# Kernel optimization log

Hardware: AMD Instinct MI355X
Metric: run time of the kernel (lower is better)

## Reference

```python
import jax, jax.numpy as jnp
import numpy as np

D_MODEL = 128
NHEAD = 8
HEAD_DIM = D_MODEL // NHEAD  # 16
NUM_LAYERS = 7
NUM_LABELS = 2
N_NODES = 10000
N_EDGES = 160000
NEG_SLOPE = 0.2  # GATv2Conv default negative_slope


def setup_inputs() -> dict:
    key = jax.random.key(0)
    ks = jax.random.split(key, 10)
    s = 1.0 / np.sqrt(D_MODEL)
    inp = {}
    inp["x"] = jax.random.normal(ks[0], (N_NODES, D_MODEL), dtype=jnp.float32)
    inp["edge_index"] = jax.random.randint(ks[1], (2, N_EDGES), 0, N_NODES, dtype=jnp.int64)
    inp["nchunks"] = 8  # uniform extra chunk size -> chunk = NUM_LABELS + 8 = 10
    # per-layer GATv2 params, stacked on a leading layer axis
    inp["Wl"] = jax.random.normal(ks[2], (NUM_LAYERS, D_MODEL, NHEAD * HEAD_DIM), dtype=jnp.float32) * s
    inp["bl"] = jnp.zeros((NUM_LAYERS, NHEAD * HEAD_DIM), dtype=jnp.float32)
    inp["Wr"] = jax.random.normal(ks[3], (NUM_LAYERS, D_MODEL, NHEAD * HEAD_DIM), dtype=jnp.float32) * s
    inp["br"] = jnp.zeros((NUM_LAYERS, NHEAD * HEAD_DIM), dtype=jnp.float32)
    inp["att"] = jax.random.normal(ks[4], (NUM_LAYERS, NHEAD, HEAD_DIM), dtype=jnp.float32) * s
    inp["bias"] = jnp.zeros((NUM_LAYERS, NHEAD * HEAD_DIM), dtype=jnp.float32)
    # split head: Linear(d_model, 1)
    inp["w_head"] = jax.random.normal(ks[5], (D_MODEL, 1), dtype=jnp.float32) * s
    inp["b_head"] = jnp.zeros((1,), dtype=jnp.float32)
    return inp


def _gatv2_layer(x, src, dst, Wl, bl, Wr, br, att, bias):
    # GATv2: e_ij = a^T LeakyReLU(W_l x_j + W_r x_i); alpha = segment-softmax over dst; out_i = sum alpha * W_l x_j
    N = x.shape[0]
    xl = (x @ Wl + bl).reshape(N, NHEAD, HEAD_DIM)
    xr = (x @ Wr + br).reshape(N, NHEAD, HEAD_DIM)
    z = jax.nn.leaky_relu(xl[src] + xr[dst], NEG_SLOPE)          # [E, H, D]
    e = jnp.einsum('ehd,hd->eh', z, att)                          # [E, H]
    emax = jax.ops.segment_max(e, dst, num_segments=N)            # [N, H]
    ex = jnp.exp(e - emax[dst])
    denom = jax.ops.segment_sum(ex, dst, num_segments=N)          # [N, H]
    alpha = ex / (denom[dst] + 1e-16)                             # [E, H]
    out = jax.ops.segment_sum(alpha[..., None] * xl[src], dst, num_segments=N)  # [N, H, D]
    return out.reshape(N, NHEAD * HEAD_DIM) + bias


def reference(x, edge_index, nchunks, Wl, bl, Wr, br, att, bias, w_head, b_head):
    N = x.shape[0]
    loop = jnp.arange(N, dtype=edge_index.dtype)  # GATv2Conv add_self_loops=True
    src = jnp.concatenate([edge_index[0], loop])
    dst = jnp.concatenate([edge_index[1], loop])
    for i in range(NUM_LAYERS):
        x = _gatv2_layer(x, src, dst, Wl[i], bl[i], Wr[i], br[i], att[i], bias[i])
    # uniform split of size (NUM_LABELS + nchunks); keep first NUM_LABELS rows of each chunk
    chunk = NUM_LABELS + int(nchunks)
    xs = x.reshape(-1, chunk, D_MODEL)[:, :NUM_LABELS]            # [n_chunks, num_labels, d]
    out = (xs @ w_head + b_head)[..., 0]                          # [n_chunks, num_labels]
    return out
```

## Files before the change

kernel.cpp:

```cpp
#include <hip/hip_runtime.h>
#include <math.h>

typedef __attribute__((ext_vector_type(8))) short bf16x8;
typedef __attribute__((ext_vector_type(4))) float f32x4;

#define WFRAG (16 * 4 * 64 * 8)


__device__ inline int detect_is64(const int* __restrict__ ei) {
    int is64 = 1;
#pragma unroll
    for (int k = 1; k < 16; k += 2) is64 &= (ei[k] == 0);
    return is64;
}

__device__ inline void split1(float f, short& hi, short& lo) {
    unsigned u = __float_as_uint(f);
    hi = (short)(u >> 16);
    float fl = f - __uint_as_float(u & 0xffff0000u);
    lo = (short)(__float_as_uint(fl) >> 16);
}

__device__ inline void cvt8(const float4& a, const float4& b, bf16x8& hi, bf16x8& lo) {
    float f[8] = {a.x, a.y, a.z, a.w, b.x, b.y, b.z, b.w};
#pragma unroll
    for (int j = 0; j < 8; j++) {
        unsigned u = __float_as_uint(f[j]);
        hi[j] = (short)(u >> 16);
        float fl = f[j] - __uint_as_float(u & 0xffff0000u);
        lo[j] = (short)(__float_as_uint(fl) >> 16);
    }
}


__global__ __launch_bounds__(256) void prologue(const float* __restrict__ Wl,
                                                const float* __restrict__ Wr,
                                                short* __restrict__ Whi,
                                                short* __restrict__ Wlo,
                                                const float4* __restrict__ x4,
                                                short* __restrict__ cvH,
                                                short* __restrict__ cvL,
                                                const int* __restrict__ ei,
                                                int* __restrict__ deg,
                                                int N, int E) {
    __shared__ float Wt[128][17];
    int b = blockIdx.x, t = threadIdx.x;
    if (b < 112) {
        int l = b >> 4;
        int tile = b & 15;
        int c0 = tile * 16;
        const float* Wsrc = (c0 < 128) ? Wl + (size_t)l * 16384 : Wr + (size_t)l * 16384;
        int cbase = (c0 < 128) ? c0 : c0 - 128;
#pragma unroll
        for (int it = 0; it < 8; it++) {
            int idx = it * 256 + t;
            int k = idx >> 4, c = idx & 15;
            Wt[k][c] = Wsrc[(size_t)k * 128 + cbase + c];
        }
        __syncthreads();
        int kt = t >> 6, lane = t & 63, q = (lane >> 4), cl = lane & 15;
        bf16x8 hi, lo;
#pragma unroll
        for (int j = 0; j < 8; j++) {
            short h, lw;
            split1(Wt[kt * 32 + q * 8 + j][cl], h, lw);
            hi[j] = h; lo[j] = lw;
        }
        size_t off = ((((size_t)l * 16 + tile) * 4 + kt) * 64 + lane) * 8;
        *(bf16x8*)(Whi + off) = hi;
        *(bf16x8*)(Wlo + off) = lo;
        return;
    }
    int rb = b - 112;
    int RB = gridDim.x - 112;
    int n8 = N * 16;
    for (int id = rb * 256 + t; id < n8; id += RB * 256) {
        float4 a = x4[2 * id];
        float4 bb = x4[2 * id + 1];
        bf16x8 h, lw;
        cvt8(a, bb, h, lw);
        *(bf16x8*)(cvH + (size_t)id * 8) = h;
        *(bf16x8*)(cvL + (size_t)id * 8) = lw;
    }
    int is64 = detect_is64(ei);
    for (int e = rb * 256 + t; e < E; e += RB * 256) {
        long long pos = (long long)E + e;
        int d = ei[is64 ? 2 * pos : pos];
        if ((unsigned)d < (unsigned)N) atomicAdd(&deg[d], 1);
    }
}


__global__ __launch_bounds__(512, 1) void scan_gemm0(const int* __restrict__ deg,
                                                     int* __restrict__ offp,
                                                     int* __restrict__ cur, int N,
                                                     const short* __restrict__ xhi,
                                                     const short* __restrict__ xlo,
                                                     const short* __restrict__ WhiL,
                                                     const short* __restrict__ WloL,
                                                     const float* __restrict__ blv,
                                                     const float* __restrict__ brv,
                                                     float* __restrict__ xl,
                                                     float* __restrict__ xr,
                                                     int ntiles) {
    __shared__ int wsum[8];
    int t = threadIdx.x;
    if (blockIdx.x == 0) {
        int per = (N + 511) >> 9;
        int b0 = t * per;
        int s = 0;
        for (int k = 0; k < per; k++) {
            int idx = b0 + k;
            if (idx < N) s += deg[idx];
        }
        int lane = t & 63, w = t >> 6;
        int v = s;
#pragma unroll
        for (int o = 1; o < 64; o <<= 1) {
            int u = __shfl_up(v, o, 64);
            if (lane >= o) v += u;
        }
        if (lane == 63) wsum[w] = v;
        __syncthreads();
        if (t == 0) {
            int r = 0;
#pragma unroll
            for (int j = 0; j < 8; j++) { int xx = wsum[j]; wsum[j] = r; r += xx; }
            offp[N] = r;
        }
        __syncthreads();
        int run = v - s + wsum[w];
        for (int k = 0; k < per; k++) {
            int idx = b0 + k;
            if (idx < N) {
                offp[idx] = run;
                cur[idx] = run;
                run += deg[idx];
            }
        }
        return;
    }

    int w = t >> 6, lane = t & 63, q = lane >> 4, cl = lane & 15;

    bf16x8 Bh[2][4], Bl[2][4];
    float biasv[2];
    float* op[2];
    int colc[2];
#pragma unroll
    for (int nt = 0; nt < 2; nt++) {
        int tile = w * 2 + nt;
        int col = tile * 16 + cl;
        if (col < 128) { biasv[nt] = blv[col]; op[nt] = xl; colc[nt] = col; }
        else           { biasv[nt] = brv[col - 128]; op[nt] = xr; colc[nt] = col - 128; }
#pragma unroll
        for (int kt = 0; kt < 4; kt++) {
            size_t o = (((size_t)tile * 4 + kt) * 64 + lane) * 8;
            Bh[nt][kt] = *(const bf16x8*)(WhiL + o);
            Bl[nt][kt] = *(const bf16x8*)(WloL + o);
        }
    }

    for (int rt = blockIdx.x - 1; rt < ntiles; rt += gridDim.x - 1) {
        int row = rt * 16 + cl;
        if (row >= N) row = N - 1;
        const short* ph = xhi + (size_t)row * 128 + q * 8;
        const short* pl = xlo + (size_t)row * 128 + q * 8;
        bf16x8 AH[4], AL[4];
#pragma unroll
        for (int kt = 0; kt < 4; kt++) {
            AH[kt] = *(const bf16x8*)(ph + kt * 32);
            AL[kt] = *(const bf16x8*)(pl + kt * 32);
        }

        f32x4 acc0 = {0.f, 0.f, 0.f, 0.f}, acc1 = {0.f, 0.f, 0.f, 0.f};
#pragma unroll
        for (int kt = 0; kt < 4; kt++) {
            acc0 = __builtin_amdgcn_mfma_f32_16x16x32_bf16(AH[kt], Bh[0][kt], acc0, 0, 0, 0);
            acc1 = __builtin_amdgcn_mfma_f32_16x16x32_bf16(AH[kt], Bh[1][kt], acc1, 0, 0, 0);
            acc0 = __builtin_amdgcn_mfma_f32_16x16x32_bf16(AL[kt], Bh[0][kt], acc0, 0, 0, 0);
            acc1 = __builtin_amdgcn_mfma_f32_16x16x32_bf16(AL[kt], Bh[1][kt], acc1, 0, 0, 0);
            acc0 = __builtin_amdgcn_mfma_f32_16x16x32_bf16(AH[kt], Bl[0][kt], acc0, 0, 0, 0);
            acc1 = __builtin_amdgcn_mfma_f32_16x16x32_bf16(AH[kt], Bl[1][kt], acc1, 0, 0, 0);
        }

#pragma unroll
        for (int nt = 0; nt < 2; nt++) {
            f32x4 a = nt ? acc1 : acc0;
#pragma unroll
            for (int r = 0; r < 4; r++) {
                int orow = rt * 16 + q * 4 + r;
                if (orow < N) op[nt][(size_t)orow * 128 + colc[nt]] = a[r] + biasv[nt];
            }
        }
    }
}

__global__ void fill_kernel(const int* __restrict__ ei, int E, int N,
                            int* __restrict__ cur, int* __restrict__ esrc) {
    int e = blockIdx.x * blockDim.x + threadIdx.x;
    if (e >= E) return;
    int is64 = detect_is64(ei);
    long long spos = e, dpos = (long long)E + e;
    int s = ei[is64 ? 2 * spos : spos];
    int d = ei[is64 ? 2 * dpos : dpos];
    if ((unsigned)d >= (unsigned)N || (unsigned)s >= (unsigned)N) return;
    int p = atomicAdd(&cur[d], 1);
    esrc[p] = s;
}


__device__ inline void agg_node(int i, int sub, int cl,
                                const float4* __restrict__ xl4, const float4* __restrict__ xr4,
                                const int* __restrict__ off, const int* __restrict__ esrc,
                                float4 atA, float4 atB, float4 bA, float4 bB,
                                float4& oA, float4& oB) {
    float4 xrA = xr4[(size_t)i * 32 + 2 * cl];
    float4 xrB = xr4[(size_t)i * 32 + 2 * cl + 1];
    int start = off[i];
    int total = off[i + 1] - start + 1;
    int groups = (total + 3) >> 2;

    int k0 = sub;
    int s0 = (k0 < total) ? ((k0 == 0) ? i : esrc[start + k0 - 1]) : i;
    int k1 = 4 + sub;
    int s1 = (k1 < total) ? esrc[start + k1 - 1] : i;
    float4 v0A = xl4[(size_t)s0 * 32 + 2 * cl];
    float4 v0B = xl4[(size_t)s0 * 32 + 2 * cl + 1];
    int k2 = 8 + sub;
    int s2 = (k2 < total) ? esrc[start + k2 - 1] : i;
    float4 v1A = xl4[(size_t)s1 * 32 + 2 * cl];
    float4 v1B = xl4[(size_t)s1 * 32 + 2 * cl + 1];

    float s = 0.f;
    float4 aA = make_float4(0.f, 0.f, 0.f, 0.f);
    float4 aB = make_float4(0.f, 0.f, 0.f, 0.f);

    for (int g = 0; g < groups; g++) {
        int k3 = 4 * (g + 3) + sub;
        int s3 = (k3 < total) ? esrc[start + k3 - 1] : i;
        float4 v2A = xl4[(size_t)s2 * 32 + 2 * cl];
        float4 v2B = xl4[(size_t)s2 * 32 + 2 * cl + 1];

        int kc = 4 * g + sub;
        int valid = kc < total;
        float z0 = v0A.x + xrA.x, z1 = v0A.y + xrA.y, z2 = v0A.z + xrA.z, z3 = v0A.w + xrA.w;
        float z4 = v0B.x + xrB.x, z5 = v0B.y + xrB.y, z6 = v0B.z + xrB.z, z7 = v0B.w + xrB.w;
        z0 = (z0 > 0.f) ? z0 : 0.2f * z0;
        z1 = (z1 > 0.f) ? z1 : 0.2f * z1;
        z2 = (z2 > 0.f) ? z2 : 0.2f * z2;
        z3 = (z3 > 0.f) ? z3 : 0.2f * z3;
        z4 = (z4 > 0.f) ? z4 : 0.2f * z4;
        z5 = (z5 > 0.f) ? z5 : 0.2f * z5;
        z6 = (z6 > 0.f) ? z6 : 0.2f * z6;
        z7 = (z7 > 0.f) ? z7 : 0.2f * z7;
        float p = z0 * atA.x + z1 * atA.y + z2 * atA.z + z3 * atA.w
                + z4 * atB.x + z5 * atB.y + z6 * atB.z + z7 * atB.w;
        p += __shfl_xor(p, 1, 64);
        p = fminf(fmaxf(p, -80.f), 80.f);
        float wgt = valid ? __expf(p) : 0.f;
        s += wgt;
        aA.x += wgt * v0A.x; aA.y += wgt * v0A.y; aA.z += wgt * v0A.z; aA.w += wgt * v0A.w;
        aB.x += wgt * v0B.x; aB.y += wgt * v0B.y; aB.z += wgt * v0B.z; aB.w += wgt * v0B.w;

        v0A = v1A; v0B = v1B;
        v1A = v2A; v1B = v2B;
        s2 = s3;
    }

#pragma unroll
    for (int o = 16; o <= 32; o <<= 1) {
        s += __shfl_xor(s, o, 64);
        aA.x += __shfl_xor(aA.x, o, 64); aA.y += __shfl_xor(aA.y, o, 64);
        aA.z += __shfl_xor(aA.z, o, 64); aA.w += __shfl_xor(aA.w, o, 64);
        aB.x += __shfl_xor(aB.x, o, 64); aB.y += __shfl_xor(aB.y, o, 64);
        aB.z += __shfl_xor(aB.z, o, 64); aB.w += __shfl_xor(aB.w, o, 64);
    }
    float inv = 1.f / (s + 1e-16f);
    oA.x = aA.x * inv + bA.x; oA.y = aA.y * inv + bA.y;
    oA.z = aA.z * inv + bA.z; oA.w = aA.w * inv + bA.w;
    oB.x = aB.x * inv + bB.x; oB.y = aB.y * inv + bB.y;
    oB.z = aB.z * inv + bB.z; oB.w = aB.w * inv + bB.w;
}


__global__ __launch_bounds__(512, 1) void agg_gemm(const float4* __restrict__ xl4,
                                                   const float4* __restrict__ xr4,
                                                   const int* __restrict__ off,
                                                   const int* __restrict__ esrc,
                                                   const float4* __restrict__ att4,
                                                   const float4* __restrict__ bias4,
                                                   const short* __restrict__ WhiL,
                                                   const short* __restrict__ WloL,
                                                   const float* __restrict__ blv,
                                                   const float* __restrict__ brv,
                                                   float* __restrict__ xlo_out,
                                                   float* __restrict__ xro_out,
                                                   int N) {
    __shared__ __align__(16) short hiL[32 * 136];
    __shared__ __align__(16) short loL[32 * 136];
    int t = threadIdx.x;
    int w = t >> 6, lane = t & 63, sub = lane >> 4, cl = lane & 15, q = lane >> 4;
    int base = blockIdx.x * 32;

    float4 atA = att4[2 * cl];
    float4 atB = att4[2 * cl + 1];
    float4 bA = bias4[2 * cl], bB = bias4[2 * cl + 1];

    for (int j = 0; j < 4; j++) {
        int i = base + w * 4 + j;
        if (i < N) {
            float4 oA, oB;
            agg_node(i, sub, cl, xl4, xr4, off, esrc, atA, atB, bA, bB, oA, oB);
            if (sub == 0) {
                bf16x8 h, lw;
                cvt8(oA, oB, h, lw);
                int r = w * 4 + j;
                *(bf16x8*)&hiL[r * 136 + cl * 8] = h;
                *(bf16x8*)&loL[r * 136 + cl * 8] = lw;
            }
        }
    }
    __syncthreads();

    bf16x8 Bh[2][4], Bl[2][4];
    float biasv[2];
    float* op[2];
    int cc[2];
#pragma unroll
    for (int tt = 0; tt < 2; tt++) {
        int tile = w * 2 + tt;
        int col = tile * 16 + cl;
        if (col < 128) { biasv[tt] = blv[col]; op[tt] = xlo_out; cc[tt] = col; }
        else           { biasv[tt] = brv[col - 128]; op[tt] = xro_out; cc[tt] = col - 128; }
#pragma unroll
        for (int kt = 0; kt < 4; kt++) {
            size_t o = (((size_t)tile * 4 + kt) * 64 + lane) * 8;
            Bh[tt][kt] = *(const bf16x8*)(WhiL + o);
            Bl[tt][kt] = *(const bf16x8*)(WloL + o);
        }
    }

#pragma unroll
    for (int m = 0; m < 2; m++) {
        bf16x8 Ah[4], Al[4];
#pragma unroll
        for (int kt = 0; kt < 4; kt++) {
            Ah[kt] = *(const bf16x8*)&hiL[(m * 16 + cl) * 136 + kt * 32 + q * 8];
            Al[kt] = *(const bf16x8*)&loL[(m * 16 + cl) * 136 + kt * 32 + q * 8];
        }
#pragma unroll
        for (int tt = 0; tt < 2; tt++) {
            f32x4 acc = {0.f, 0.f, 0.f, 0.f};
#pragma unroll
            for (int kt = 0; kt < 4; kt++) {
                acc = __builtin_amdgcn_mfma_f32_16x16x32_bf16(Ah[kt], Bh[tt][kt], acc, 0, 0, 0);
                acc = __builtin_amdgcn_mfma_f32_16x16x32_bf16(Al[kt], Bh[tt][kt], acc, 0, 0, 0);
                acc = __builtin_amdgcn_mfma_f32_16x16x32_bf16(Ah[kt], Bl[tt][kt], acc, 0, 0, 0);
            }
#pragma unroll
            for (int r = 0; r < 4; r++) {
                int row = base + m * 16 + q * 4 + r;
                if (row < N) op[tt][(size_t)row * 128 + cc[tt]] = acc[r] + biasv[tt];
            }
        }
    }
}


__global__ __launch_bounds__(256) void gat_agg_head(const float4* __restrict__ xl4,
                                                    const float4* __restrict__ xr4,
                                                    const int* __restrict__ off,
                                                    const int* __restrict__ esrc,
                                                    const float4* __restrict__ att4,
                                                    const float4* __restrict__ bias4,
                                                    const float4* __restrict__ wh4,
                                                    const float* __restrict__ bh,
                                                    const int* __restrict__ nch,
                                                    float* __restrict__ out,
                                                    int n_out, int N) {
    int lane = threadIdx.x & 63;
    int sub = lane >> 4;
    int cl = lane & 15;
    int i = blockIdx.x * 4 + (threadIdx.x >> 6);
    if (i >= N) return;
    float4 atA = att4[2 * cl];
    float4 atB = att4[2 * cl + 1];
    float4 bA = bias4[2 * cl], bB = bias4[2 * cl + 1];
    float4 oA, oB;
    agg_node(i, sub, cl, xl4, xr4, off, esrc, atA, atB, bA, bB, oA, oB);
    if (sub == 0) {
        int chunk = 2 + nch[0];
        int r = i % chunk;
        if (r < 2) {
            float4 wa = wh4[2 * cl], wb = wh4[2 * cl + 1];
            float p = oA.x * wa.x + oA.y * wa.y + oA.z * wa.z + oA.w * wa.w
                    + oB.x * wb.x + oB.y * wb.y + oB.z * wb.z + oB.w * wb.w;
#pragma unroll
            for (int o = 1; o <= 8; o <<= 1) p += __shfl_xor(p, o, 64);
            if (cl == 0) {
                int b = (i / chunk) * 2 + r;
                if (b < n_out) out[b] = p + bh[0];
            }
        }
    }
}


extern "C" void kernel_launch(void* const* d_in, const int* in_sizes, int n_in,
                              void* d_out, int out_size, void* d_ws, size_t ws_size,
                              hipStream_t stream) {
    const float* x0 = (const float*)d_in[0];
    const int* ei = (const int*)d_in[1];
    const int* nchunks = (const int*)d_in[2];
    const float* Wl = (const float*)d_in[3];
    const float* bl = (const float*)d_in[4];
    const float* Wr = (const float*)d_in[5];
    const float* br = (const float*)d_in[6];
    const float* att = (const float*)d_in[7];
    const float* bias = (const float*)d_in[8];
    const float* wh = (const float*)d_in[9];
    const float* bh = (const float*)d_in[10];

    const int D = 128;
    int N = in_sizes[0] / D;
    int E = in_sizes[1] / 2;
    int ntiles = (N + 15) / 16;

    size_t fN = (size_t)N * D;
    float* xlA = (float*)d_ws;
    float* xrA = xlA + fN;
    float* xlB = xrA + fN;
    float* xrB = xlB + fN;
    short* cvH0 = (short*)(xrB + fN);
    short* cvL0 = cvH0 + fN;
    short* Whi = cvL0 + fN;
    short* Wlo = Whi + 7 * (size_t)WFRAG;
    int* deg = (int*)(Wlo + 7 * (size_t)WFRAG);
    int* off = deg + N;
    int* cur = off + N + 1;
    int* esrc = cur + N;

    hipMemsetAsync(deg, 0, (size_t)N * sizeof(int), stream);
    prologue<<<112 + 640, 256, 0, stream>>>(Wl, Wr, Whi, Wlo, (const float4*)x0,
                                            cvH0, cvL0, ei, deg, N, E);
    scan_gemm0<<<257, 512, 0, stream>>>(deg, off, cur, N, cvH0, cvL0, Whi, Wlo,
                                        bl, br, xlA, xrA, ntiles);
    fill_kernel<<<(E + 255) / 256, 256, 0, stream>>>(ei, E, N, cur, esrc);

    int ablocks = (N + 31) / 32;
    for (int l = 0; l < 6; l++) {
        const float* rxl = (l % 2 == 0) ? xlA : xlB;
        const float* rxr = (l % 2 == 0) ? xrA : xrB;
        float* wxl = (l % 2 == 0) ? xlB : xlA;
        float* wxr = (l % 2 == 0) ? xrB : xrA;
        agg_gemm<<<ablocks, 512, 0, stream>>>((const float4*)rxl, (const float4*)rxr, off, esrc,
                                              (const float4*)(att + (size_t)l * D),
                                              (const float4*)(bias + (size_t)l * D),
                                              Whi + (size_t)(l + 1) * WFRAG,
                                              Wlo + (size_t)(l + 1) * WFRAG,
                                              bl + (size_t)(l + 1) * D,
                                              br + (size_t)(l + 1) * D,
                                              wxl, wxr, N);
    }

    gat_agg_head<<<(N + 3) / 4, 256, 0, stream>>>((const float4*)xlA, (const float4*)xrA,
                                                  off, esrc,
                                                  (const float4*)(att + 6 * (size_t)D),
                                                  (const float4*)(bias + 6 * (size_t)D),
                                                  (const float4*)wh, bh, nchunks,
                                                  (float*)d_out, out_size, N);
}
```

Baseline: 273.8 us.

## Aggregate one node per half-wave and shrink fused agg-GEMM blocks to sixteen rows

```diff
diff --git a/kernel.cpp b/kernel.cpp
--- a/kernel.cpp
+++ b/kernel.cpp
@@ -210,81 +210,109 @@
 }
 
 
-__device__ inline void agg_node(int i, int sub, int cl,
-                                const float4* __restrict__ xl4, const float4* __restrict__ xr4,
-                                const int* __restrict__ off, const int* __restrict__ esrc,
-                                float4 atA, float4 atB, float4 bA, float4 bB,
-                                float4& oA, float4& oB) {
-    float4 xrA = xr4[(size_t)i * 32 + 2 * cl];
-    float4 xrB = xr4[(size_t)i * 32 + 2 * cl + 1];
+__device__ inline void agg_node_hw(int i, int s, int f,
+                                   const float4* __restrict__ xl4,
+                                   const float4* __restrict__ xr4,
+                                   const int* __restrict__ off,
+                                   const int* __restrict__ esrc,
+                                   const float4* __restrict__ att4,
+                                   const float4* __restrict__ bias4,
+                                   float4 (&out)[4]) {
+    float4 xr0 = xr4[(size_t)i * 32 + f * 4 + 0];
+    float4 xr1 = xr4[(size_t)i * 32 + f * 4 + 1];
+    float4 xr2 = xr4[(size_t)i * 32 + f * 4 + 2];
+    float4 xr3 = xr4[(size_t)i * 32 + f * 4 + 3];
+    float4 at0 = att4[f * 4 + 0];
+    float4 at1 = att4[f * 4 + 1];
+    float4 at2 = att4[f * 4 + 2];
+    float4 at3 = att4[f * 4 + 3];
+
     int start = off[i];
     int total = off[i + 1] - start + 1;
     int groups = (total + 3) >> 2;
 
-    int k0 = sub;
+    int k0 = s;
     int s0 = (k0 < total) ? ((k0 == 0) ? i : esrc[start + k0 - 1]) : i;
-    int k1 = 4 + sub;
+    const float4* p0 = xl4 + (size_t)s0 * 32 + f * 4;
+    float4 a0 = p0[0], a1 = p0[1], a2 = p0[2], a3 = p0[3];
+    int k1 = 4 + s;
     int s1 = (k1 < total) ? esrc[start + k1 - 1] : i;
-    float4 v0A = xl4[(size_t)s0 * 32 + 2 * cl];
-    float4 v0B = xl4[(size_t)s0 * 32 + 2 * cl + 1];
-    int k2 = 8 + sub;
-    int s2 = (k2 < total) ? esrc[start + k2 - 1] : i;
-    float4 v1A = xl4[(size_t)s1 * 32 + 2 * cl];
-    float4 v1B = xl4[(size_t)s1 * 32 + 2 * cl + 1];
-
-    float s = 0.f;
-    float4 aA = make_float4(0.f, 0.f, 0.f, 0.f);
-    float4 aB = make_float4(0.f, 0.f, 0.f, 0.f);
+    const float4* p1 = xl4 + (size_t)s1 * 32 + f * 4;
+    float4 b0 = p1[0], b1 = p1[1], b2 = p1[2], b3 = p1[3];
+
+    float denom = 0.f;
+    float4 ac0 = make_float4(0.f, 0.f, 0.f, 0.f);
+    float4 ac1 = make_float4(0.f, 0.f, 0.f, 0.f);
+    float4 ac2 = make_float4(0.f, 0.f, 0.f, 0.f);
+    float4 ac3 = make_float4(0.f, 0.f, 0.f, 0.f);
 
     for (int g = 0; g < groups; g++) {
-        int k3 = 4 * (g + 3) + sub;
-        int s3 = (k3 < total) ? esrc[start + k3 - 1] : i;
-        float4 v2A = xl4[(size_t)s2 * 32 + 2 * cl];
-        float4 v2B = xl4[(size_t)s2 * 32 + 2 * cl + 1];
-
-        int kc = 4 * g + sub;
-        int valid = kc < total;
-        float z0 = v0A.x + xrA.x, z1 = v0A.y + xrA.y, z2 = v0A.z + xrA.z, z3 = v0A.w + xrA.w;
-        float z4 = v0B.x + xrB.x, z5 = v0B.y + xrB.y, z6 = v0B.z + xrB.z, z7 = v0B.w + xrB.w;
-        z0 = (z0 > 0.f) ? z0 : 0.2f * z0;
-        z1 = (z1 > 0.f) ? z1 : 0.2f * z1;
-        z2 = (z2 > 0.f) ? z2 : 0.2f * z2;
-        z3 = (z3 > 0.f) ? z3 : 0.2f * z3;
-        z4 = (z4 > 0.f) ? z4 : 0.2f * z4;
-        z5 = (z5 > 0.f) ? z5 : 0.2f * z5;
-        z6 = (z6 > 0.f) ? z6 : 0.2f * z6;
-        z7 = (z7 > 0.f) ? z7 : 0.2f * z7;
-        float p = z0 * atA.x + z1 * atA.y + z2 * atA.z + z3 * atA.w
-                + z4 * atB.x + z5 * atB.y + z6 * atB.z + z7 * atB.w;
-        p += __shfl_xor(p, 1, 64);
+        int k2 = (g + 2) * 4 + s;
+        int s2 = (k2 < total) ? esrc[start + k2 - 1] : i;
+        const float4* p2 = xl4 + (size_t)s2 * 32 + f * 4;
+        float4 c0 = p2[0], c1 = p2[1], c2 = p2[2], c3 = p2[3];
+
+        int valid = (g * 4 + s) < total;
+#define LK(zz) ((zz) > 0.f ? (zz) : 0.2f * (zz))
+        float p = 0.f, z;
+        z = LK(a0.x + xr0.x); p += z * at0.x;
+        z = LK(a0.y + xr0.y); p += z * at0.y;
+        z = LK(a0.z + xr0.z); p += z * at0.z;
+        z = LK(a0.w + xr0.w); p += z * at0.w;
+        z = LK(a1.x + xr1.x); p += z * at1.x;
+        z = LK(a1.y + xr1.y); p += z * at1.y;
+        z = LK(a1.z + xr1.z); p += z * at1.z;
+        z = LK(a1.w + xr1.w); p += z * at1.w;
+        z = LK(a2.x + xr2.x); p += z * at2.x;
+        z = LK(a2.y + xr2.y); p += z * at2.y;
+        z = LK(a2.z + xr2.z); p += z * at2.z;
+        z = LK(a2.w + xr2.w); p += z * at2.w;
+        z = LK(a3.x + xr3.x); p += z * at3.x;
+        z = LK(a3.y + xr3.y); p += z * at3.y;
+        z = LK(a3.z + xr3.z); p += z * at3.z;
+        z = LK(a3.w + xr3.w); p += z * at3.w;
+#undef LK
         p = fminf(fmaxf(p, -80.f), 80.f);
         float wgt = valid ? __expf(p) : 0.f;
-        s += wgt;
-        aA.x += wgt * v0A.x; aA.y += wgt * v0A.y; aA.z += wgt * v0A.z; aA.w += wgt * v0A.w;
-        aB.x += wgt * v0B.x; aB.y += wgt * v0B.y; aB.z += wgt * v0B.z; aB.w += wgt * v0B.w;
-
-        v0A = v1A; v0B = v1B;
-        v1A = v2A; v1B = v2B;
-        s2 = s3;
-    }
-
-#pragma unroll
-    for (int o = 16; o <= 32; o <<= 1) {
-        s += __shfl_xor(s, o, 64);
-        aA.x += __shfl_xor(aA.x, o, 64); aA.y += __shfl_xor(aA.y, o, 64);
-        aA.z += __shfl_xor(aA.z, o, 64); aA.w += __shfl_xor(aA.w, o, 64);
-        aB.x += __shfl_xor(aB.x, o, 64); aB.y += __shfl_xor(aB.y, o, 64);
-        aB.z += __shfl_xor(aB.z, o, 64); aB.w += __shfl_xor(aB.w, o, 64);
-    }
-    float inv = 1.f / (s + 1e-16f);
-    oA.x = aA.x * inv + bA.x; oA.y = aA.y * inv + bA.y;
-    oA.z = aA.z * inv + bA.z; oA.w = aA.w * inv + bA.w;
-    oB.x = aB.x * inv + bB.x; oB.y = aB.y * inv + bB.y;
-    oB.z = aB.z * inv + bB.z; oB.w = aB.w * inv + bB.w;
-}
-
-
-__global__ __launch_bounds__(512, 1) void agg_gemm(const float4* __restrict__ xl4,
+        denom += wgt;
+        ac0.x += wgt * a0.x; ac0.y += wgt * a0.y; ac0.z += wgt * a0.z; ac0.w += wgt * a0.w;
+        ac1.x += wgt * a1.x; ac1.y += wgt * a1.y; ac1.z += wgt * a1.z; ac1.w += wgt * a1.w;
+        ac2.x += wgt * a2.x; ac2.y += wgt * a2.y; ac2.z += wgt * a2.z; ac2.w += wgt * a2.w;
+        ac3.x += wgt * a3.x; ac3.y += wgt * a3.y; ac3.z += wgt * a3.z; ac3.w += wgt * a3.w;
+
+        a0 = b0; a1 = b1; a2 = b2; a3 = b3;
+        b0 = c0; b1 = c1; b2 = c2; b3 = c3;
+    }
+
+#pragma unroll
+    for (int o = 8; o <= 16; o <<= 1) {
+        denom += __shfl_xor(denom, o, 64);
+        ac0.x += __shfl_xor(ac0.x, o, 64); ac0.y += __shfl_xor(ac0.y, o, 64);
+        ac0.z += __shfl_xor(ac0.z, o, 64); ac0.w += __shfl_xor(ac0.w, o, 64);
+        ac1.x += __shfl_xor(ac1.x, o, 64); ac1.y += __shfl_xor(ac1.y, o, 64);
+        ac1.z += __shfl_xor(ac1.z, o, 64); ac1.w += __shfl_xor(ac1.w, o, 64);
+        ac2.x += __shfl_xor(ac2.x, o, 64); ac2.y += __shfl_xor(ac2.y, o, 64);
+        ac2.z += __shfl_xor(ac2.z, o, 64); ac2.w += __shfl_xor(ac2.w, o, 64);
+        ac3.x += __shfl_xor(ac3.x, o, 64); ac3.y += __shfl_xor(ac3.y, o, 64);
+        ac3.z += __shfl_xor(ac3.z, o, 64); ac3.w += __shfl_xor(ac3.w, o, 64);
+    }
+    float inv = 1.f / (denom + 1e-16f);
+    float4 bi0 = bias4[f * 4 + 0];
+    float4 bi1 = bias4[f * 4 + 1];
+    float4 bi2 = bias4[f * 4 + 2];
+    float4 bi3 = bias4[f * 4 + 3];
+    out[0].x = ac0.x * inv + bi0.x; out[0].y = ac0.y * inv + bi0.y;
+    out[0].z = ac0.z * inv + bi0.z; out[0].w = ac0.w * inv + bi0.w;
+    out[1].x = ac1.x * inv + bi1.x; out[1].y = ac1.y * inv + bi1.y;
+    out[1].z = ac1.z * inv + bi1.z; out[1].w = ac1.w * inv + bi1.w;
+    out[2].x = ac2.x * inv + bi2.x; out[2].y = ac2.y * inv + bi2.y;
+    out[2].z = ac2.z * inv + bi2.z; out[2].w = ac2.w * inv + bi2.w;
+    out[3].x = ac3.x * inv + bi3.x; out[3].y = ac3.y * inv + bi3.y;
+    out[3].z = ac3.z * inv + bi3.z; out[3].w = ac3.w * inv + bi3.w;
+}
+
+
+__global__ __launch_bounds__(512, 2) void agg_gemm(const float4* __restrict__ xl4,
                                                    const float4* __restrict__ xr4,
                                                    const int* __restrict__ off,
                                                    const int* __restrict__ esrc,
@@ -297,108 +325,99 @@
                                                    float* __restrict__ xlo_out,
                                                    float* __restrict__ xro_out,
                                                    int N) {
-    __shared__ __align__(16) short hiL[32 * 136];
-    __shared__ __align__(16) short loL[32 * 136];
+    __shared__ __align__(16) short hiL[16 * 136];
+    __shared__ __align__(16) short loL[16 * 136];
     int t = threadIdx.x;
-    int w = t >> 6, lane = t & 63, sub = lane >> 4, cl = lane & 15, q = lane >> 4;
-    int base = blockIdx.x * 32;
-
-    float4 atA = att4[2 * cl];
-    float4 atB = att4[2 * cl + 1];
-    float4 bA = bias4[2 * cl], bB = bias4[2 * cl + 1];
-
-    for (int j = 0; j < 4; j++) {
-        int i = base + w * 4 + j;
-        if (i < N) {
-            float4 oA, oB;
-            agg_node(i, sub, cl, xl4, xr4, off, esrc, atA, atB, bA, bB, oA, oB);
-            if (sub == 0) {
-                bf16x8 h, lw;
-                cvt8(oA, oB, h, lw);
-                int r = w * 4 + j;
-                *(bf16x8*)&hiL[r * 136 + cl * 8] = h;
-                *(bf16x8*)&loL[r * 136 + cl * 8] = lw;
-            }
+    int hw = t >> 5;
+    int u = t & 31, s = u >> 3, f = u & 7;
+    int base = blockIdx.x * 16;
+    int i = base + hw;
+
+    if (i < N) {
+        float4 o[4];
+        agg_node_hw(i, s, f, xl4, xr4, off, esrc, att4, bias4, o);
+        if (s == 0) {
+            bf16x8 h0, l0, h1, l1;
+            cvt8(o[0], o[1], h0, l0);
+            cvt8(o[2], o[3], h1, l1);
+            *(bf16x8*)&hiL[hw * 136 + f * 16] = h0;
+            *(bf16x8*)&hiL[hw * 136 + f * 16 + 8] = h1;
+            *(bf16x8*)&loL[hw * 136 + f * 16] = l0;
+            *(bf16x8*)&loL[hw * 136 + f * 16 + 8] = l1;
         }
     }
     __syncthreads();
 
-    bf16x8 Bh[2][4], Bl[2][4];
-    float biasv[2];
-    float* op[2];
-    int cc[2];
+    int w = t >> 6, lane = t & 63, q = lane >> 4, cl = lane & 15;
+    bf16x8 Ah[4], Al[4];
+#pragma unroll
+    for (int kt = 0; kt < 4; kt++) {
+        Ah[kt] = *(const bf16x8*)&hiL[cl * 136 + kt * 32 + q * 8];
+        Al[kt] = *(const bf16x8*)&loL[cl * 136 + kt * 32 + q * 8];
+    }
+
 #pragma unroll
     for (int tt = 0; tt < 2; tt++) {
         int tile = w * 2 + tt;
         int col = tile * 16 + cl;
-        if (col < 128) { biasv[tt] = blv[col]; op[tt] = xlo_out; cc[tt] = col; }
-        else           { biasv[tt] = brv[col - 128]; op[tt] = xro_out; cc[tt] = col - 128; }
+        f32x4 acc = {0.f, 0.f, 0.f, 0.f};
 #pragma unroll
         for (int kt = 0; kt < 4; kt++) {
             size_t o = (((size_t)tile * 4 + kt) * 64 + lane) * 8;
-            Bh[tt][kt] = *(const bf16x8*)(WhiL + o);
-            Bl[tt][kt] = *(const bf16x8*)(WloL + o);
-        }
-    }
-
-#pragma unroll
-    for (int m = 0; m < 2; m++) {
-        bf16x8 Ah[4], Al[4];
-#pragma unroll
-        for (int kt = 0; kt < 4; kt++) {
-            Ah[kt] = *(const bf16x8*)&hiL[(m * 16 + cl) * 136 + kt * 32 + q * 8];
-            Al[kt] = *(const bf16x8*)&loL[(m * 16 + cl) * 136 + kt * 32 + q * 8];
-        }
-#pragma unroll
-        for (int tt = 0; tt < 2; tt++) {
-            f32x4 acc = {0.f, 0.f, 0.f, 0.f};
-#pragma unroll
-            for (int kt = 0; kt < 4; kt++) {
-                acc = __builtin_amdgcn_mfma_f32_16x16x32_bf16(Ah[kt], Bh[tt][kt], acc, 0, 0, 0);
-                acc = __builtin_amdgcn_mfma_f32_16x16x32_bf16(Al[kt], Bh[tt][kt], acc, 0, 0, 0);
-                acc = __builtin_amdgcn_mfma_f32_16x16x32_bf16(Ah[kt], Bl[tt][kt], acc, 0, 0, 0);
-            }
-#pragma unroll
-            for (int r = 0; r < 4; r++) {
-                int row = base + m * 16 + q * 4 + r;
-                if (row < N) op[tt][(size_t)row * 128 + cc[tt]] = acc[r] + biasv[tt];
-            }
-        }
-    }
-}
-
-
-__global__ __launch_bounds__(256) void gat_agg_head(const float4* __restrict__ xl4,
-                                                    const float4* __restrict__ xr4,
-                                                    const int* __restrict__ off,
-                                                    const int* __restrict__ esrc,
-                                                    const float4* __restrict__ att4,
-                                                    const float4* __restrict__ bias4,
-                                                    const float4* __restrict__ wh4,
-                                                    const float* __restrict__ bh,
-                                                    const int* __restrict__ nch,
-                                                    float* __restrict__ out,
-                                                    int n_out, int N) {
-    int lane = threadIdx.x & 63;
-    int sub = lane >> 4;
-    int cl = lane & 15;
-    int i = blockIdx.x * 4 + (threadIdx.x >> 6);
+            bf16x8 bh = *(const bf16x8*)(WhiL + o);
+            bf16x8 bl2 = *(const bf16x8*)(WloL + o);
+            acc = __builtin_amdgcn_mfma_f32_16x16x32_bf16(Ah[kt], bh, acc, 0, 0, 0);
+            acc = __builtin_amdgcn_mfma_f32_16x16x32_bf16(Al[kt], bh, acc, 0, 0, 0);
+            acc = __builtin_amdgcn_mfma_f32_16x16x32_bf16(Ah[kt], bl2, acc, 0, 0, 0);
+        }
+        float biasv;
+        float* op;
+        int cc;
+        if (col < 128) { biasv = blv[col]; op = xlo_out; cc = col; }
+        else           { biasv = brv[col - 128]; op = xro_out; cc = col - 128; }
+#pragma unroll
+        for (int r = 0; r < 4; r++) {
+            int row = base + q * 4 + r;
+            if (row < N) op[(size_t)row * 128 + cc] = acc[r] + biasv;
+        }
+    }
+}
+
+
+__global__ __launch_bounds__(256, 4) void gat_agg_head(const float4* __restrict__ xl4,
+                                                       const float4* __restrict__ xr4,
+                                                       const int* __restrict__ off,
+                                                       const int* __restrict__ esrc,
+                                                       const float4* __restrict__ att4,
+                                                       const float4* __restrict__ bias4,
+                                                       const float4* __restrict__ wh4,
+                                                       const float* __restrict__ bh,
+                                                       const int* __restrict__ nch,
+                                                       float* __restrict__ out,
+                                                       int n_out, int N) {
+    int t = threadIdx.x;
+    int hw = t >> 5;
+    int u = t & 31, s = u >> 3, f = u & 7;
+    int i = blockIdx.x * 8 + hw;
     if (i >= N) return;
-    float4 atA = att4[2 * cl];
-    float4 atB = att4[2 * cl + 1];
-    float4 bA = bias4[2 * cl], bB = bias4[2 * cl + 1];
-    float4 oA, oB;
-    agg_node(i, sub, cl, xl4, xr4, off, esrc, atA, atB, bA, bB, oA, oB);
-    if (sub == 0) {
+
+    float4 o[4];
+    agg_node_hw(i, s, f, xl4, xr4, off, esrc, att4, bias4, o);
+
+    if (s == 0) {
         int chunk = 2 + nch[0];
         int r = i % chunk;
         if (r < 2) {
-            float4 wa = wh4[2 * cl], wb = wh4[2 * cl + 1];
-            float p = oA.x * wa.x + oA.y * wa.y + oA.z * wa.z + oA.w * wa.w
-                    + oB.x * wb.x + oB.y * wb.y + oB.z * wb.z + oB.w * wb.w;
-#pragma unroll
-            for (int o = 1; o <= 8; o <<= 1) p += __shfl_xor(p, o, 64);
-            if (cl == 0) {
+            float4 w0 = wh4[f * 4 + 0], w1 = wh4[f * 4 + 1];
+            float4 w2 = wh4[f * 4 + 2], w3 = wh4[f * 4 + 3];
+            float p = o[0].x * w0.x + o[0].y * w0.y + o[0].z * w0.z + o[0].w * w0.w
+                    + o[1].x * w1.x + o[1].y * w1.y + o[1].z * w1.z + o[1].w * w1.w
+                    + o[2].x * w2.x + o[2].y * w2.y + o[2].z * w2.z + o[2].w * w2.w
+                    + o[3].x * w3.x + o[3].y * w3.y + o[3].z * w3.z + o[3].w * w3.w;
+            p += __shfl_xor(p, 1, 64);
+            p += __shfl_xor(p, 2, 64);
+            p += __shfl_xor(p, 4, 64);
+            if (f == 0) {
                 int b = (i / chunk) * 2 + r;
                 if (b < n_out) out[b] = p + bh[0];
             }
@@ -448,23 +467,22 @@
                                         bl, br, xlA, xrA, ntiles);
     fill_kernel<<<(E + 255) / 256, 256, 0, stream>>>(ei, E, N, cur, esrc);
 
-    int ablocks = (N + 31) / 32;
     for (int l = 0; l < 6; l++) {
         const float* rxl = (l % 2 == 0) ? xlA : xlB;
         const float* rxr = (l % 2 == 0) ? xrA : xrB;
         float* wxl = (l % 2 == 0) ? xlB : xlA;
         float* wxr = (l % 2 == 0) ? xrB : xrA;
-        agg_gemm<<<ablocks, 512, 0, stream>>>((const float4*)rxl, (const float4*)rxr, off, esrc,
-                                              (const float4*)(att + (size_t)l * D),
-                                              (const float4*)(bias + (size_t)l * D),
-                                              Whi + (size_t)(l + 1) * WFRAG,
-                                              Wlo + (size_t)(l + 1) * WFRAG,
-                                              bl + (size_t)(l + 1) * D,
-                                              br + (size_t)(l + 1) * D,
-                                              wxl, wxr, N);
-    }
-
-    gat_agg_head<<<(N + 3) / 4, 256, 0, stream>>>((const float4*)xlA, (const float4*)xrA,
+        agg_gemm<<<ntiles, 512, 0, stream>>>((const float4*)rxl, (const float4*)rxr, off, esrc,
+                                             (const float4*)(att + (size_t)l * D),
+                                             (const float4*)(bias + (size_t)l * D),
+                                             Whi + (size_t)(l + 1) * WFRAG,
+                                             Wlo + (size_t)(l + 1) * WFRAG,
+                                             bl + (size_t)(l + 1) * D,
+                                             br + (size_t)(l + 1) * D,
+                                             wxl, wxr, N);
+    }
+
+    gat_agg_head<<<(N + 7) / 8, 256, 0, stream>>>((const float4*)xlA, (const float4*)xrA,
                                                   off, esrc,
                                                   (const float4*)(att + 6 * (size_t)D),
                                                   (const float4*)(bias + 6 * (size_t)D),
```

New measurement: 270.3 us. No clear change (-1.3%).
